# Kernel tuning notes

Measured on AMD Instinct MI355X. Metric: run time of the kernel, lower is better.

The kernel has to match this reference:

```python
import jax, jax.numpy as jnp
import numpy as np

HIDDEN = 512
NUM_HEADS = 8
HEAD = HIDDEN // NUM_HEADS
TOP_K = 64
NEG = -1e9


def setup_inputs() -> dict:
    key = jax.random.key(0)
    ks = jax.random.split(key, 12)
    B, Q, S = 2, 2048, 4096
    sc = 0.02
    return {
        "main_input": jax.random.normal(ks[0], (B, Q, HIDDEN), jnp.float32),
        "side_input": jax.random.normal(ks[1], (S, HIDDEN), jnp.float32),
        "att_mask": jax.random.randint(ks[2], (B, Q, S), 0, 2, jnp.int32),
        "Wq": jax.random.normal(ks[3], (HIDDEN, HIDDEN), jnp.float32) * sc,
        "bq": jnp.zeros((HIDDEN,), jnp.float32),
        "Wk": jax.random.normal(ks[4], (HIDDEN, HIDDEN), jnp.float32) * sc,
        "bk": jnp.zeros((HIDDEN,), jnp.float32),
        "Wv": jax.random.normal(ks[5], (HIDDEN, HIDDEN), jnp.float32) * sc,
        "bv": jnp.zeros((HIDDEN,), jnp.float32),
        "Wo": jax.random.normal(ks[6], (HIDDEN, HIDDEN), jnp.float32) * sc,
        "bo": jnp.zeros((HIDDEN,), jnp.float32),
    }


def reference(main_input, side_input, att_mask, Wq, bq, Wk, bk, Wv, bv, Wo, bo):
    B, Qlen, _ = main_input.shape
    S = side_input.shape[0]
    # multi-head projections; side K/V shared across the whole batch
    q = (main_input @ Wq + bq).reshape(B, Qlen, NUM_HEADS, HEAD)
    k = (side_input @ Wk + bk).reshape(S, NUM_HEADS, HEAD)
    v = (side_input @ Wv + bv).reshape(S, NUM_HEADS, HEAD)
    # scores: [B, H, Q, S]
    scores = jnp.einsum("bqhd,khd->bhqk", q, k) / jnp.sqrt(jnp.asarray(HEAD, q.dtype))
    # attention mask (0 = masked)
    mask = att_mask[:, None, :, :].astype(scores.dtype)  # [B,1,Q,S]
    scores = scores + (1.0 - mask) * NEG
    # top-k restriction: keep only the TOP_K largest scores per query row
    thresh = jax.lax.top_k(scores, TOP_K)[0][..., -1:]  # kth largest
    scores = jnp.where(scores >= thresh, scores, NEG)
    probs = jax.nn.softmax(scores, axis=-1)
    ctx = jnp.einsum("bhqk,khd->bqhd", probs, v).reshape(B, Qlen, HIDDEN)
    return ctx @ Wo + bo
```

## Files before the change

### kernel.cpp

```cpp
#include <hip/hip_runtime.h>
#include <stdint.h>

typedef uint32_t u32;
typedef unsigned long long u64;

#define NEGV (-1e9f)
#define NCAND 16
#define LISTCAP 256

__device__ __forceinline__ u32 f2ord(float f) {
  u32 x = __float_as_uint(f);
  return (x & 0x80000000u) ? ~x : (x | 0x80000000u);
}
__device__ __forceinline__ float ord2f(u32 u) {
  u32 x = (u & 0x80000000u) ? (u ^ 0x80000000u) : ~u;
  return __uint_as_float(x);
}

__global__ __launch_bounds__(256)
void pack_mask(const int* __restrict__ mask, u64* __restrict__ mbits) {
  int w = blockIdx.x * 256 + threadIdx.x;
  const int4* p = (const int4*)(mask + (size_t)w * 64);
  u64 bits = 0;
#pragma unroll
  for (int j = 0; j < 16; ++j) {
    int4 m = p[j];
    if (m.x) bits |= 1ull << (j * 4 + 0);
    if (m.y) bits |= 1ull << (j * 4 + 1);
    if (m.z) bits |= 1ull << (j * 4 + 2);
    if (m.w) bits |= 1ull << (j * 4 + 3);
  }
  mbits[w] = bits;
}

__global__ __launch_bounds__(256)
void gemm_bias(const float* __restrict__ A, const float* __restrict__ W,
               const float* __restrict__ bias, float* __restrict__ C) {
  __shared__ float As[16][68];
  __shared__ float Bs[16][64];
  const int tid = threadIdx.x;
  const int tx = tid & 15, ty = tid >> 4;
  const int n0 = blockIdx.x << 6, m0 = blockIdx.y << 6;
  float c[4][4] = {};
  for (int k0 = 0; k0 < 512; k0 += 16) {
    {
      const int row = tid >> 2, kp = (tid & 3) << 2;
      float4 av = *(const float4*)&A[(size_t)(m0 + row) * 512 + k0 + kp];
      As[kp + 0][row] = av.x;
      As[kp + 1][row] = av.y;
      As[kp + 2][row] = av.z;
      As[kp + 3][row] = av.w;
      const int kk = tid >> 4, np = (tid & 15) << 2;
      *(float4*)&Bs[kk][np] = *(const float4*)&W[(size_t)(k0 + kk) * 512 + n0 + np];
    }
    __syncthreads();
#pragma unroll
    for (int kk = 0; kk < 16; ++kk) {
      float4 a = *(const float4*)&As[kk][ty << 2];
      float4 b = *(const float4*)&Bs[kk][tx << 2];
      c[0][0] += a.x * b.x; c[0][1] += a.x * b.y; c[0][2] += a.x * b.z; c[0][3] += a.x * b.w;
      c[1][0] += a.y * b.x; c[1][1] += a.y * b.y; c[1][2] += a.y * b.z; c[1][3] += a.y * b.w;
      c[2][0] += a.z * b.x; c[2][1] += a.z * b.y; c[2][2] += a.z * b.z; c[2][3] += a.z * b.w;
      c[3][0] += a.w * b.x; c[3][1] += a.w * b.y; c[3][2] += a.w * b.z; c[3][3] += a.w * b.w;
    }
    __syncthreads();
  }
  float4 bv = *(const float4*)&bias[n0 + (tx << 2)];
#pragma unroll
  for (int i = 0; i < 4; ++i) {
    float4 o;
    o.x = c[i][0] + bv.x; o.y = c[i][1] + bv.y;
    o.z = c[i][2] + bv.z; o.w = c[i][3] + bv.w;
    *(float4*)&C[(size_t)(m0 + (ty << 2) + i) * 512 + n0 + (tx << 2)] = o;
  }
}

__global__ __launch_bounds__(256)
void gemm_bias_T(const float* __restrict__ A, const float* __restrict__ W,
                 const float* __restrict__ bias, float* __restrict__ CT, int qsh) {
  __shared__ float As[16][68];
  __shared__ float Bs[16][64];
  const int tid = threadIdx.x;
  const int tx = tid & 15, ty = tid >> 4;
  const int n0 = blockIdx.x << 6, m0 = blockIdx.y << 6;
  float c[4][4] = {};
  for (int k0 = 0; k0 < 512; k0 += 16) {
    {
      const int row = tid >> 2, kp = (tid & 3) << 2;
      float4 av = *(const float4*)&A[(size_t)(m0 + row) * 512 + k0 + kp];
      As[kp + 0][row] = av.x;
      As[kp + 1][row] = av.y;
      As[kp + 2][row] = av.z;
      As[kp + 3][row] = av.w;
      const int kk = tid >> 4, np = (tid & 15) << 2;
      *(float4*)&Bs[kk][np] = *(const float4*)&W[(size_t)(k0 + kk) * 512 + n0 + np];
    }
    __syncthreads();
#pragma unroll
    for (int kk = 0; kk < 16; ++kk) {
      float4 a = *(const float4*)&As[kk][ty << 2];
      float4 b = *(const float4*)&Bs[kk][tx << 2];
      c[0][0] += a.x * b.x; c[0][1] += a.x * b.y; c[0][2] += a.x * b.z; c[0][3] += a.x * b.w;
      c[1][0] += a.y * b.x; c[1][1] += a.y * b.y; c[1][2] += a.y * b.z; c[1][3] += a.y * b.w;
      c[2][0] += a.z * b.x; c[2][1] += a.z * b.y; c[2][2] += a.z * b.z; c[2][3] += a.z * b.w;
      c[3][0] += a.w * b.x; c[3][1] += a.w * b.y; c[3][2] += a.w * b.z; c[3][3] += a.w * b.w;
    }
    __syncthreads();
  }
  float4 bv = *(const float4*)&bias[n0 + (tx << 2)];
  float bvv[4] = {bv.x, bv.y, bv.z, bv.w};
  const int qlen = 1 << qsh;
  const int qmask = qlen - 1;
#pragma unroll
  for (int i = 0; i < 4; ++i) {
#pragma unroll
    for (int j = 0; j < 4; ++j) {
      float val = c[i][j] + bvv[j];
      int m = m0 + (ty << 2) + i;
      int n = n0 + (tx << 2) + j;
      int h = n >> 6, d = n & 63;
      int bb = m >> qsh, q = m & qmask;
      CT[(((size_t)bb * 8 + h) * 64 + d) * qlen + q] = val;
    }
  }
}

__global__ __launch_bounds__(256)
void score_kernel(const float* __restrict__ qT, const float* __restrict__ kT,
                  const u64* __restrict__ mbits, float* __restrict__ sbuf,
                  float* __restrict__ segmax, int sl0) {
  __shared__ float Qs[32][128];
  __shared__ float Ks[32][128];
  const int sl = sl0 + blockIdx.z;
  const int b = sl >> 3, h = sl & 7;
  const int s0 = blockIdx.x << 7, q0 = blockIdx.y << 7;
  const int tid = threadIdx.x;
  const float* qbase = qT + (size_t)sl * 64 * 2048 + q0;
  const float* kbase = kT + (size_t)h * 64 * 4096 + s0;
  const int tx = tid & 15, ty = tid >> 4;
  float4* Qf = (float4*)&Qs[0][0];
  float4* Kf = (float4*)&Ks[0][0];
  float c[8][8] = {};
  for (int half = 0; half < 2; ++half) {
#pragma unroll
    for (int u = 0; u < 4; ++u) {
      int i = (u << 8) + tid;
      int row = i >> 5, col = (i & 31) << 2;
      Qf[i] = *(const float4*)(qbase + (size_t)(half * 32 + row) * 2048 + col);
      Kf[i] = *(const float4*)(kbase + (size_t)(half * 32 + row) * 4096 + col);
    }
    __syncthreads();
#pragma unroll 4
    for (int g = 0; g < 8; ++g) {
      const int kk = g << 2;
      float qa[8][4], kb[8][4];
#pragma unroll
      for (int t = 0; t < 4; ++t) {
        float4 qv0 = *(const float4*)&Qs[kk + t][(ty << 3) + 0];
        float4 qv1 = *(const float4*)&Qs[kk + t][(ty << 3) + 4];
        qa[0][t] = qv0.x; qa[1][t] = qv0.y; qa[2][t] = qv0.z; qa[3][t] = qv0.w;
        qa[4][t] = qv1.x; qa[5][t] = qv1.y; qa[6][t] = qv1.z; qa[7][t] = qv1.w;
        float4 kv0 = *(const float4*)&Ks[kk + t][(tx << 2)];
        float4 kv1 = *(const float4*)&Ks[kk + t][64 + (tx << 2)];
        kb[0][t] = kv0.x; kb[1][t] = kv0.y; kb[2][t] = kv0.z; kb[3][t] = kv0.w;
        kb[4][t] = kv1.x; kb[5][t] = kv1.y; kb[6][t] = kv1.z; kb[7][t] = kv1.w;
      }
#pragma unroll
      for (int i = 0; i < 8; ++i)
#pragma unroll
        for (int j = 0; j < 8; ++j)
          c[i][j] += qa[i][0] * kb[j][0] + qa[i][1] * kb[j][1]
                   + qa[i][2] * kb[j][2] + qa[i][3] * kb[j][3];
    }
    __syncthreads();
  }
  float* srow = sbuf + ((size_t)blockIdx.z * 2048 + q0) * 4096 + s0;
  const u64* mrow = mbits + ((size_t)(b * 2048 + q0)) * 64 + (s0 >> 6);
#pragma unroll
  for (int i = 0; i < 8; ++i) {
    const int row = (ty << 3) + i;
    u64 wA = mrow[(size_t)row * 64];
    u64 wB = mrow[(size_t)row * 64 + 1];
    float4 o0, o1;
    o0.x = ((wA >> ((tx << 2) + 0)) & 1) ? c[i][0] * 0.125f : NEGV;
    o0.y = ((wA >> ((tx << 2) + 1)) & 1) ? c[i][1] * 0.125f : NEGV;
    o0.z = ((wA >> ((tx << 2) + 2)) & 1) ? c[i][2] * 0.125f : NEGV;
    o0.w = ((wA >> ((tx << 2) + 3)) & 1) ? c[i][3] * 0.125f : NEGV;
    o1.x = ((wB >> ((tx << 2) + 0)) & 1) ? c[i][4] * 0.125f : NEGV;
    o1.y = ((wB >> ((tx << 2) + 1)) & 1) ? c[i][5] * 0.125f : NEGV;
    o1.z = ((wB >> ((tx << 2) + 2)) & 1) ? c[i][6] * 0.125f : NEGV;
    o1.w = ((wB >> ((tx << 2) + 3)) & 1) ? c[i][7] * 0.125f : NEGV;
    *(float4*)&srow[(size_t)row * 4096 + (tx << 2)] = o0;
    *(float4*)&srow[(size_t)row * 4096 + 64 + (tx << 2)] = o1;
    float m0 = fmaxf(fmaxf(o0.x, o0.y), fmaxf(o0.z, o0.w));
    float m1 = fmaxf(fmaxf(o1.x, o1.y), fmaxf(o1.z, o1.w));
#pragma unroll
    for (int off = 4; off; off >>= 1) {
      m0 = fmaxf(m0, __shfl_xor(m0, off, 64));
      m1 = fmaxf(m1, __shfl_xor(m1, off, 64));
    }
    if ((tx & 7) == 0) {
      size_t sg = ((size_t)blockIdx.z * 2048 + q0 + row) * 128 + (s0 >> 5) + (tx >> 3);
      segmax[sg] = m0;
      segmax[sg + 2] = m1;
    }
  }
}

__global__ __launch_bounds__(256)
void topk_ctx_kernel(const float* __restrict__ sbuf, const float* __restrict__ segmax,
                     const float* __restrict__ vbuf, float* __restrict__ ctxbuf,
                     int sl0) {
  const int sl = sl0 + blockIdx.y;
  const int b = sl >> 3, h = sl & 7;
  const int w = threadIdx.x >> 6, lane = threadIdx.x & 63;
  const int qi = (blockIdx.x << 2) + w;
  __shared__ u64 cand_lds[4][NCAND][64];
  u64* list = &cand_lds[w][0][0];
  const u64 lmask_lt = (1ull << lane) - 1ull;
  const u32 ordneg = f2ord(NEGV);

  const float* srow = sbuf + ((size_t)blockIdx.y * 2048 + qi) * 4096;

  float2 smv = *(const float2*)(segmax + ((size_t)blockIdx.y * 2048 + qi) * 128 + (lane << 1));
  u32 so0 = f2ord(smv.x), so1 = f2ord(smv.y);
  u32 mxo = so0 > so1 ? so0 : so1;
  u32 mno = so0 < so1 ? so0 : so1;
#pragma unroll
  for (int off = 32; off; off >>= 1) {
    u32 a = (u32)__shfl_xor((int)mxo, off, 64);
    u32 c = (u32)__shfl_xor((int)mno, off, 64);
    mxo = a > mxo ? a : mxo;
    mno = c < mno ? c : mno;
  }
  const float fm = ord2f(mxo);
  {
    u32 lo = mno, hi = mxo + 1;
    while (hi - lo > 1) {
      u32 mid = lo + ((hi - lo) >> 1);
      int c = __popcll(__ballot(so0 >= mid)) + __popcll(__ballot(so1 >= mid));
      if (c >= 64) lo = mid; else hi = mid;
    }
    mno = lo;
  }
  const u32 ordT = mno;
  const float Tf = ord2f(ordT);

  int cnt = 0;
  const float* lbase = srow + (lane << 6);
#pragma unroll
  for (int reg = 0; reg < 2; ++reg) {
    bool active = (reg == 0) ? (smv.x >= Tf) : (smv.y >= Tf);
    if (active) {
      const float* rb = lbase + (reg << 5);
      float4 v0 = *(const float4*)(rb + 0);
      float4 v1 = *(const float4*)(rb + 4);
      float4 v2 = *(const float4*)(rb + 8);
      float4 v3 = *(const float4*)(rb + 12);
      float4 v4 = *(const float4*)(rb + 16);
      float4 v5 = *(const float4*)(rb + 20);
      float4 v6 = *(const float4*)(rb + 24);
      float4 v7 = *(const float4*)(rb + 28);
      float xs[32] = {v0.x, v0.y, v0.z, v0.w, v1.x, v1.y, v1.z, v1.w,
                      v2.x, v2.y, v2.z, v2.w, v3.x, v3.y, v3.z, v3.w,
                      v4.x, v4.y, v4.z, v4.w, v5.x, v5.y, v5.z, v5.w,
                      v6.x, v6.y, v6.z, v6.w, v7.x, v7.y, v7.z, v7.w};
#pragma unroll
      for (int cc = 0; cc < 32; ++cc) {
        if (xs[cc] >= Tf) {
          if (cnt < NCAND) {
            int sidx = (lane << 6) + (reg << 5) + cc;
            cand_lds[w][cnt][lane] = ((u64)f2ord(xs[cc]) << 32) | (u32)sidx;
          }
          cnt++;
        }
      }
    }
  }
  const bool fb = (__ballot(cnt > NCAND) != 0ull);

  float esum = 0.f;
  int nsel = 0;
  bool meanpath = false;

  if (!fb) {
    u32 co[NCAND];
#pragma unroll
    for (int j = 0; j < NCAND; ++j)
      co[j] = (j < cnt) ? ((const u32*)&cand_lds[w][j][lane])[1] : 0u;
    u32 lo = ordT, hi = mxo + 1;
    while (hi - lo > 1) {
      u32 mid = lo + ((hi - lo) >> 1);
      int c = 0;
#pragma unroll
      for (int j = 0; j < NCAND; ++j)
        c += __popcll(__ballot(co[j] >= mid));
      if (c >= 64) lo = mid; else hi = mid;
    }
    int base = 0;
#pragma unroll
    for (int j = 0; j < NCAND; ++j) {
      bool pred = (j < cnt) && (co[j] >= lo);
      u64 m = __ballot(pred);
      int ofs = base + __popcll(m & lmask_lt);
      if (pred && ofs < LISTCAP) {
        u64 cj = cand_lds[w][j][lane];
        float ev = __expf(ord2f((u32)(cj >> 32)) - fm);
        list[ofs] = ((u64)((u32)cj) << 32) | (u64)__float_as_uint(ev);
        esum += ev;
      }
      base += (int)__popcll(m);
    }
    nsel = base < LISTCAP ? base : LISTCAP;
  } else {
    u32 lo = ordT, hi = mxo + 1;
    while (hi - lo > 1) {
      u32 mid = lo + ((hi - lo) >> 1);
      float midf = ord2f(mid);
      int c = 0;
      for (int j = 0; j < 16; ++j) {
        float4 v = *(const float4*)(srow + (j << 8) + (lane << 2));
        c += __popcll(__ballot(v.x >= midf)) + __popcll(__ballot(v.y >= midf)) +
             __popcll(__ballot(v.z >= midf)) + __popcll(__ballot(v.w >= midf));
      }
      if (c >= 64) lo = mid; else hi = mid;
    }
    const float thrf = ord2f(lo);
    int base = 0;
    for (int j = 0; j < 16; ++j) {
      float4 v = *(const float4*)(srow + (j << 8) + (lane << 2));
      float xs[4] = {v.x, v.y, v.z, v.w};
#pragma unroll
      for (int cpos = 0; cpos < 4; ++cpos) {
        float x = xs[cpos];
        bool pred = (x >= thrf) && (x != NEGV);
        u64 m = __ballot(pred);
        int ofs = base + __popcll(m & lmask_lt);
        if (pred && ofs < LISTCAP) {
          int sidx = (j << 8) + (lane << 2) + cpos;
          float ev = __expf(x - fm);
          list[ofs] = ((u64)(u32)sidx << 32) | (u64)__float_as_uint(ev);
          esum += ev;
        }
        base += (int)__popcll(m);
      }
    }
    nsel = base < LISTCAP ? base : LISTCAP;
    if (base == 0) meanpath = true;
  }

#pragma unroll
  for (int off = 32; off; off >>= 1) esum += __shfl_xor(esum, off, 64);
  const float* vb = vbuf + h * 64 + lane;
  float outv;
  if (!meanpath) {
    const float rs = 1.0f / esum;
    int pad = (8 - (nsel & 7)) & 7;
    if (lane < pad && nsel + lane < LISTCAP) list[nsel + lane] = 0;
    int n8 = nsel + pad;
    if (n8 > LISTCAP) n8 = LISTCAP;
    float a0 = 0.f, a1 = 0.f, a2 = 0.f, a3 = 0.f;
    float a4 = 0.f, a5 = 0.f, a6 = 0.f, a7 = 0.f;
    for (int g = 0; g < n8; g += 8) {
      u64 p0 = list[g + 0], p1 = list[g + 1], p2 = list[g + 2], p3 = list[g + 3];
      u64 p4 = list[g + 4], p5 = list[g + 5], p6 = list[g + 6], p7 = list[g + 7];
      a0 += __uint_as_float((u32)p0) * vb[(size_t)(p0 >> 32) * 512];
      a1 += __uint_as_float((u32)p1) * vb[(size_t)(p1 >> 32) * 512];
      a2 += __uint_as_float((u32)p2) * vb[(size_t)(p2 >> 32) * 512];
      a3 += __uint_as_float((u32)p3) * vb[(size_t)(p3 >> 32) * 512];
      a4 += __uint_as_float((u32)p4) * vb[(size_t)(p4 >> 32) * 512];
      a5 += __uint_as_float((u32)p5) * vb[(size_t)(p5 >> 32) * 512];
      a6 += __uint_as_float((u32)p6) * vb[(size_t)(p6 >> 32) * 512];
      a7 += __uint_as_float((u32)p7) * vb[(size_t)(p7 >> 32) * 512];
    }
    outv = (((a0 + a1) + (a2 + a3)) + ((a4 + a5) + (a6 + a7))) * rs;
  } else {
    float acc = 0.f;
    for (int s = 0; s < 4096; ++s) acc += vb[(size_t)s * 512];
    outv = acc * (1.0f / 4096.0f);
  }
  ctxbuf[((size_t)(b * 2048 + qi)) * 512 + h * 64 + lane] = outv;
}

extern "C" void kernel_launch(void* const* d_in, const int* in_sizes, int n_in,
                              void* d_out, int out_size, void* d_ws, size_t ws_size,
                              hipStream_t stream) {
  const float* main_in = (const float*)d_in[0];
  const float* side_in = (const float*)d_in[1];
  const int*   mask    = (const int*)d_in[2];
  const float* Wq = (const float*)d_in[3];
  const float* bq = (const float*)d_in[4];
  const float* Wk = (const float*)d_in[5];
  const float* bk = (const float*)d_in[6];
  const float* Wv = (const float*)d_in[7];
  const float* bv = (const float*)d_in[8];
  const float* Wo = (const float*)d_in[9];
  const float* bo = (const float*)d_in[10];
  float* out = (float*)d_out;

  char* ws = (char*)d_ws;
  float* qT   = (float*)(ws);
  float* kT   = (float*)(ws + ((size_t)8 << 20));
  float* vbuf = (float*)(ws + ((size_t)16 << 20));
  float* ctxb = (float*)(ws + ((size_t)24 << 20));
  u64* mbits  = (u64*)(ws + ((size_t)32 << 20));
  const size_t base = (size_t)34 << 20;
  const size_t sliceb = (size_t)2048 * 4096 * 4;
  const size_t segb   = (size_t)2048 * 128 * 4;
  const size_t per = sliceb + segb;

  int nz = 1;
  if (ws_size > base + per) {
    size_t m = (ws_size - base) / per;
    nz = (int)(m > 4 ? 4 : m);
  }
  float* sbuf = (float*)(ws + base);
  float* smax = (float*)(ws + base + (size_t)nz * sliceb);

  pack_mask<<<1024, 256, 0, stream>>>(mask, mbits);
  gemm_bias_T<<<dim3(8, 64), 256, 0, stream>>>(main_in, Wq, bq, qT, 11);
  gemm_bias_T<<<dim3(8, 64), 256, 0, stream>>>(side_in, Wk, bk, kT, 12);
  gemm_bias  <<<dim3(8, 64), 256, 0, stream>>>(side_in, Wv, bv, vbuf);

  for (int sl0 = 0; sl0 < 16; sl0 += nz) {
    int z = nz < (16 - sl0) ? nz : (16 - sl0);
    score_kernel   <<<dim3(32, 16, z), 256, 0, stream>>>(qT, kT, mbits, sbuf, smax, sl0);
    topk_ctx_kernel<<<dim3(512, z), 256, 0, stream>>>(sbuf, smax, vbuf, ctxb, sl0);
  }

  gemm_bias<<<dim3(8, 64), 256, 0, stream>>>(ctxb, Wo, bo, out);
}
```

Measured before the change: 760.4 us.

## Compact top-k candidates via prefix scan, use direct-to-LDS loads, widen gather unroll

The score GEMM tile loads now use global_load_lds so data goes straight to shared memory without passing through registers. In top-k selection, per-lane candidate counts are prefix-scanned and compacted into a dense shared list, so the threshold search ballots over 4 registers instead of 16 per-lane slots. The per-lane candidate cap drops from 16 to 8, which may send more rows to the slow full-row fallback path. The V gather loop is unrolled to 16 accumulators to expose more memory-level parallelism.

```diff
diff --git a/kernel.cpp b/kernel.cpp
--- a/kernel.cpp
+++ b/kernel.cpp
@@ -5,8 +5,8 @@
 typedef unsigned long long u64;
 
 #define NEGV (-1e9f)
-#define NCAND 16
-#define LISTCAP 256
+#define NCAND 8
+#define SCAP 256
 
 __device__ __forceinline__ u32 f2ord(float f) {
   u32 x = __float_as_uint(f);
@@ -15,6 +15,12 @@
 __device__ __forceinline__ float ord2f(u32 u) {
   u32 x = (u & 0x80000000u) ? (u ^ 0x80000000u) : ~u;
   return __uint_as_float(x);
+}
+
+__device__ __forceinline__ void gl_lds16(const void* g, void* l) {
+  __builtin_amdgcn_global_load_lds(
+      (const __attribute__((address_space(1))) u32*)g,
+      (__attribute__((address_space(3))) u32*)l, 16, 0, 0);
 }
 
 __global__ __launch_bounds__(256)
@@ -146,8 +152,8 @@
     for (int u = 0; u < 4; ++u) {
       int i = (u << 8) + tid;
       int row = i >> 5, col = (i & 31) << 2;
-      Qf[i] = *(const float4*)(qbase + (size_t)(half * 32 + row) * 2048 + col);
-      Kf[i] = *(const float4*)(kbase + (size_t)(half * 32 + row) * 4096 + col);
+      gl_lds16(qbase + (size_t)(half * 32 + row) * 2048 + col, &Qf[i]);
+      gl_lds16(kbase + (size_t)(half * 32 + row) * 4096 + col, &Kf[i]);
     }
     __syncthreads();
 #pragma unroll 4
@@ -216,9 +222,9 @@
   const int w = threadIdx.x >> 6, lane = threadIdx.x & 63;
   const int qi = (blockIdx.x << 2) + w;
   __shared__ u64 cand_lds[4][NCAND][64];
-  u64* list = &cand_lds[w][0][0];
+  __shared__ u64 list_s[4][SCAP + 4];
+  u64* list = list_s[w];
   const u64 lmask_lt = (1ull << lane) - 1ull;
-  const u32 ordneg = f2ord(NEGV);
 
   const float* srow = sbuf + ((size_t)blockIdx.y * 2048 + qi) * 4096;
 
@@ -277,41 +283,58 @@
       }
     }
   }
-  const bool fb = (__ballot(cnt > NCAND) != 0ull);
+  int inc = cnt;
+#pragma unroll
+  for (int off = 1; off < 64; off <<= 1) {
+    int t = __shfl_up(inc, off, 64);
+    if (lane >= off) inc += t;
+  }
+  const int total = __shfl(inc, 63, 64);
+  const int off0 = inc - cnt;
+  const bool fb = (__ballot(cnt > NCAND) != 0ull) || (total > SCAP);
 
   float esum = 0.f;
   int nsel = 0;
   bool meanpath = false;
 
   if (!fb) {
-    u32 co[NCAND];
-#pragma unroll
-    for (int j = 0; j < NCAND; ++j)
-      co[j] = (j < cnt) ? ((const u32*)&cand_lds[w][j][lane])[1] : 0u;
+#pragma unroll
+    for (int t = 0; t < NCAND; ++t)
+      if (t < cnt) list[off0 + t] = cand_lds[w][t][lane];
+    asm volatile("s_waitcnt lgkmcnt(0)" ::: "memory");
+    u64 cj[4];
+    u32 co[4];
+#pragma unroll
+    for (int r = 0; r < 4; ++r) {
+      int idx = lane + (r << 6);
+      cj[r] = (idx < total) ? list[idx] : 0;
+      co[r] = (u32)(cj[r] >> 32);
+    }
     u32 lo = ordT, hi = mxo + 1;
     while (hi - lo > 1) {
       u32 mid = lo + ((hi - lo) >> 1);
       int c = 0;
 #pragma unroll
-      for (int j = 0; j < NCAND; ++j)
-        c += __popcll(__ballot(co[j] >= mid));
+      for (int r = 0; r < 4; ++r)
+        c += __popcll(__ballot(co[r] >= mid));
       if (c >= 64) lo = mid; else hi = mid;
     }
+    asm volatile("s_waitcnt lgkmcnt(0)" ::: "memory");
+    const u64 tp = (u64)lo << 32;
     int base = 0;
 #pragma unroll
-    for (int j = 0; j < NCAND; ++j) {
-      bool pred = (j < cnt) && (co[j] >= lo);
+    for (int r = 0; r < 4; ++r) {
+      bool pred = cj[r] >= tp;
       u64 m = __ballot(pred);
       int ofs = base + __popcll(m & lmask_lt);
-      if (pred && ofs < LISTCAP) {
-        u64 cj = cand_lds[w][j][lane];
-        float ev = __expf(ord2f((u32)(cj >> 32)) - fm);
-        list[ofs] = ((u64)((u32)cj) << 32) | (u64)__float_as_uint(ev);
+      if (pred && ofs < SCAP) {
+        float ev = __expf(ord2f(co[r]) - fm);
+        list[ofs] = ((u64)((u32)cj[r]) << 32) | (u64)__float_as_uint(ev);
         esum += ev;
       }
       base += (int)__popcll(m);
     }
-    nsel = base < LISTCAP ? base : LISTCAP;
+    nsel = base < SCAP ? base : SCAP;
   } else {
     u32 lo = ordT, hi = mxo + 1;
     while (hi - lo > 1) {
@@ -336,7 +359,7 @@
         bool pred = (x >= thrf) && (x != NEGV);
         u64 m = __ballot(pred);
         int ofs = base + __popcll(m & lmask_lt);
-        if (pred && ofs < LISTCAP) {
+        if (pred && ofs < SCAP) {
           int sidx = (j << 8) + (lane << 2) + cpos;
           float ev = __expf(x - fm);
           list[ofs] = ((u64)(u32)sidx << 32) | (u64)__float_as_uint(ev);
@@ -345,7 +368,7 @@
         base += (int)__popcll(m);
       }
     }
-    nsel = base < LISTCAP ? base : LISTCAP;
+    nsel = base < SCAP ? base : SCAP;
     if (base == 0) meanpath = true;
   }
 
@@ -355,25 +378,24 @@
   float outv;
   if (!meanpath) {
     const float rs = 1.0f / esum;
-    int pad = (8 - (nsel & 7)) & 7;
-    if (lane < pad && nsel + lane < LISTCAP) list[nsel + lane] = 0;
-    int n8 = nsel + pad;
-    if (n8 > LISTCAP) n8 = LISTCAP;
-    float a0 = 0.f, a1 = 0.f, a2 = 0.f, a3 = 0.f;
-    float a4 = 0.f, a5 = 0.f, a6 = 0.f, a7 = 0.f;
-    for (int g = 0; g < n8; g += 8) {
-      u64 p0 = list[g + 0], p1 = list[g + 1], p2 = list[g + 2], p3 = list[g + 3];
-      u64 p4 = list[g + 4], p5 = list[g + 5], p6 = list[g + 6], p7 = list[g + 7];
-      a0 += __uint_as_float((u32)p0) * vb[(size_t)(p0 >> 32) * 512];
-      a1 += __uint_as_float((u32)p1) * vb[(size_t)(p1 >> 32) * 512];
-      a2 += __uint_as_float((u32)p2) * vb[(size_t)(p2 >> 32) * 512];
-      a3 += __uint_as_float((u32)p3) * vb[(size_t)(p3 >> 32) * 512];
-      a4 += __uint_as_float((u32)p4) * vb[(size_t)(p4 >> 32) * 512];
-      a5 += __uint_as_float((u32)p5) * vb[(size_t)(p5 >> 32) * 512];
-      a6 += __uint_as_float((u32)p6) * vb[(size_t)(p6 >> 32) * 512];
-      a7 += __uint_as_float((u32)p7) * vb[(size_t)(p7 >> 32) * 512];
-    }
-    outv = (((a0 + a1) + (a2 + a3)) + ((a4 + a5) + (a6 + a7))) * rs;
+    int pad = (16 - (nsel & 15)) & 15;
+    if (lane < pad && nsel + lane < SCAP) list[nsel + lane] = 0;
+    int n16 = nsel + pad;
+    if (n16 > SCAP) n16 = SCAP;
+    asm volatile("s_waitcnt lgkmcnt(0)" ::: "memory");
+    float a[16];
+#pragma unroll
+    for (int t = 0; t < 16; ++t) a[t] = 0.f;
+    for (int g = 0; g < n16; g += 16) {
+#pragma unroll
+      for (int t = 0; t < 16; ++t) {
+        u64 p = list[g + t];
+        a[t] += __uint_as_float((u32)p) * vb[(size_t)(p >> 32) * 512];
+      }
+    }
+    float s0 = ((a[0] + a[1]) + (a[2] + a[3])) + ((a[4] + a[5]) + (a[6] + a[7]));
+    float s1 = ((a[8] + a[9]) + (a[10] + a[11])) + ((a[12] + a[13]) + (a[14] + a[15]));
+    outv = (s0 + s1) * rs;
   } else {
     float acc = 0.f;
     for (int s = 0; s < 4096; ++s) acc += vb[(size_t)s * 512];
```

Measured after the change: 789.0 us. +3.8%, slower.
